# Kernel optimization log

Measured on AMD Instinct MI355X. Metric: run time of the kernel, lower is better.

Reference implementation:

```python
import jax, jax.numpy as jnp
import numpy as np

FEAT = 256
NUM_ATOMS = np.array([2048, 1536, 1024, 2048, 512, 1792, 1280, 2048], dtype=np.int32)
B = len(NUM_ATOMS)
N = int(NUM_ATOMS.sum())          # 12288 total atoms
MAXN = int(NUM_ATOMS.max())       # 2048
# Static segment bookkeeping (num_atoms is structural, not data)
_OFFSETS = np.concatenate([[0], np.cumsum(NUM_ATOMS)[:-1]])
SEG = np.repeat(np.arange(B), NUM_ATOMS)            # [N] graph id per atom
POS = np.arange(N) - _OFFSETS[SEG]                  # [N] position within graph
VALID = np.arange(MAXN)[None, :] < NUM_ATOMS[:, None]  # [B, MAXN] key mask


def setup_inputs() -> dict:
    key = jax.random.key(0)
    k1, k2 = jax.random.split(key)
    s = jax.random.normal(k1, (N, FEAT), jnp.float32)
    # dense: feat_dim -> 3*feat_dim, with bias
    W = jax.random.normal(k2, (FEAT, 3 * FEAT), jnp.float32) / np.float32(np.sqrt(FEAT))
    b = jnp.zeros((3 * FEAT,), jnp.float32)
    num_atoms = jnp.asarray(NUM_ATOMS)
    return {"s": s, "W": W, "b": b, "num_atoms": num_atoms}


def _pad(X):
    # scatter flat [N, FEAT] atoms into padded [B, MAXN, FEAT]
    return jnp.zeros((B, MAXN, FEAT), X.dtype).at[SEG, POS].set(X)


def reference(s, W, b, num_atoms):
    qkv = s @ W + b                          # [N, 3*FEAT]
    Q, K, V = jnp.split(qkv, 3, axis=-1)     # each [N, FEAT]
    Qp, Kp, Vp = _pad(Q), _pad(K), _pad(V)   # [B, MAXN, FEAT]
    scale = np.float32(1.0 / np.sqrt(FEAT))
    scores = jnp.einsum('bqd,bkd->bqk', Qp, Kp) * scale   # [B, MAXN, MAXN]
    scores = jnp.where(VALID[:, None, :], scores, -jnp.inf)  # mask padded keys
    att = jax.nn.softmax(scores, axis=-1)
    out = jnp.einsum('bqk,bkd->bqd', att, Vp)             # [B, MAXN, FEAT]
    return out[SEG, POS]                                   # back to flat [N, FEAT]
```

## Files before the change

kernel.cpp:

```cpp
#include <hip/hip_runtime.h>

typedef __attribute__((ext_vector_type(8))) short short8;
typedef __attribute__((ext_vector_type(4))) short s16x4;
typedef __attribute__((ext_vector_type(4))) float f32x4;

#define MFMA16(a,b,c) __builtin_amdgcn_mfma_f32_16x16x32_bf16((a),(b),(c),0,0,0)

__device__ __forceinline__ ushort f2bf(float f){ union{float f; unsigned u;} v; v.f=f; unsigned r=v.u + 0x7fffu + ((v.u>>16)&1u); return (ushort)(r>>16); }
__device__ __forceinline__ float bf2f(ushort u){ union{unsigned u; float f;} v; v.u = ((unsigned)u)<<16; return v.f; }

__global__ void __launch_bounds__(256) prep(const float* __restrict__ S,
    ushort* __restrict__ Sb, const float* __restrict__ W, ushort* __restrict__ Wt)
{
    __shared__ __align__(16) ushort tile[64*72];
    const int t = threadIdx.x;
    if (blockIdx.x < 1024){
        const int tid = blockIdx.x*256 + t;
#pragma unroll
        for (int r=0;r<3;r++){
            const int idx = tid + r*262144;
            f32x4 v = ((const f32x4*)S)[idx];
            s16x4 o;
            o[0]=(short)f2bf(v[0]); o[1]=(short)f2bf(v[1]);
            o[2]=(short)f2bf(v[2]); o[3]=(short)f2bf(v[3]);
            ((s16x4*)Sb)[idx] = o;
        }
    } else {
        const int i = blockIdx.x - 1024;
        const int r0 = (i&3)*64, c0 = (i>>2)*64;
        const int rr = t>>2, g = (t&3)*16;
        const float* sp = W + (size_t)(r0+rr)*768 + c0 + g;
#pragma unroll
        for (int j=0;j<16;j++) tile[(g+j)*72 + rr] = f2bf(sp[j]);
        __syncthreads();
        ushort* dp = Wt + (size_t)(c0+rr)*256 + r0 + g;
        *(short8*)dp     = *(const short8*)&tile[rr*72 + g];
        *(short8*)(dp+8) = *(const short8*)&tile[rr*72 + g + 8];
    }
}

__global__ void __launch_bounds__(256) qkv_gemm(const ushort* __restrict__ Sb,
    const ushort* __restrict__ Wt, const float* __restrict__ bias,
    ushort* __restrict__ Q, ushort* __restrict__ K, ushort* __restrict__ Vt)
{
    __shared__ __align__(16) ushort Bl[64*264];
    const int t = threadIdx.x, w = t>>6, l = t&63, lr = l&15, lq = l>>4;
    const int m0 = blockIdx.x*128, n0 = blockIdx.y*64;

    const ushort* ap = Sb + (size_t)(m0 + w*32 + lr)*256 + lq*8;
    short8 sa[2][8];
#pragma unroll
    for (int g=0;g<2;g++)
#pragma unroll
        for (int kc=0;kc<8;kc++)
            sa[g][kc] = *(const short8*)(ap + g*16*256 + kc*32);

#pragma unroll
    for (int s=0;s<8;s++){
        const int u = t + s*256, row = u>>5, c8 = u&31;
        *(short8*)&Bl[row*264 + c8*8] = *(const short8*)(Wt + (size_t)(n0+row)*256 + c8*8);
    }
    __syncthreads();

    if (n0 < 512){
        f32x4 acc[2][4];
#pragma unroll
        for (int a=0;a<2;a++)
#pragma unroll
            for (int b2=0;b2<4;b2++) acc[a][b2]=(f32x4){0.f,0.f,0.f,0.f};
#pragma unroll
        for (int kc=0;kc<8;kc++){
#pragma unroll
            for (int nt=0;nt<4;nt++){
                short8 bf = *(const short8*)&Bl[(nt*16+lr)*264 + lq*8 + kc*32];
                acc[0][nt] = MFMA16(sa[0][kc], bf, acc[0][nt]);
                acc[1][nt] = MFMA16(sa[1][kc], bf, acc[1][nt]);
            }
        }
        ushort* dst = (n0 < 256) ? Q : K;
        const int colbase = n0 & 255;
#pragma unroll
        for (int nt=0;nt<4;nt++){
            float bv = bias[n0 + nt*16 + lr];
#pragma unroll
            for (int mt=0;mt<2;mt++){
                const int row = m0 + w*32 + mt*16 + lq*4;
                ushort* o = dst + (size_t)row*256 + colbase + nt*16 + lr;
#pragma unroll
                for (int i=0;i<4;i++) o[(size_t)i*256] = f2bf(acc[mt][nt][i] + bv);
            }
        }
    } else {
        const int f0 = n0 - 512;
        f32x4 acc[4][2];
#pragma unroll
        for (int a=0;a<4;a++)
#pragma unroll
            for (int b2=0;b2<2;b2++) acc[a][b2]=(f32x4){0.f,0.f,0.f,0.f};
#pragma unroll
        for (int kc=0;kc<8;kc++){
#pragma unroll
            for (int ft=0;ft<4;ft++){
                short8 af = *(const short8*)&Bl[(ft*16+lr)*264 + lq*8 + kc*32];
                acc[ft][0] = MFMA16(af, sa[0][kc], acc[ft][0]);
                acc[ft][1] = MFMA16(af, sa[1][kc], acc[ft][1]);
            }
        }
#pragma unroll
        for (int ft=0;ft<4;ft++){
#pragma unroll
            for (int at=0;at<2;at++){
                ushort* o = Vt + (size_t)(f0 + ft*16 + lq*4)*12288 + m0 + w*32 + at*16 + lr;
#pragma unroll
                for (int i=0;i<4;i++){
                    float bv = bias[512 + f0 + ft*16 + lq*4 + i];
                    o[(size_t)i*12288] = f2bf(acc[ft][at][i] + bv);
                }
            }
        }
    }
}

template<int MODE, int PL>
__global__ void __launch_bounds__(256,2) attn_partial(const ushort* __restrict__ Qb,
    const ushort* __restrict__ Kb, const ushort* __restrict__ Vt,
    void* __restrict__ Optr, float* __restrict__ Lptr)
{
    __shared__ __align__(16) ushort Kl[32*264];
    __shared__ __align__(16) ushort Vl[256*40];
    __shared__ __align__(16) ushort Pl[4][32*40];
    const int t = threadIdx.x, w = t>>6, l = t&63, lr = l&15, lq = l>>4;
    constexpr int PIECE = 1 << PL;

    const int offs[9] = {0,2048,3584,4608,6656,7168,8960,10240,12288};
    int bi = blockIdx.x, q0=0, kstart=0, kend=0, off=0, nbg=0, pbase=0, pb=0;
#pragma unroll
    for (int s=0;s<8;s++){
        const int nb = offs[s+1]-offs[s];
        const int tiles = nb>>7, pieces = (nb + PIECE-1)>>PL;
        const int items = tiles*pieces;
        if (bi >= 0 && bi < items){
            const int tile = bi / pieces, piece = bi - tile*pieces;
            q0 = offs[s] + tile*128;
            kstart = offs[s] + piece*PIECE;
            kend = min(offs[s]+nb, kstart+PIECE);
            off = offs[s]; nbg = nb; pbase = pb;
        }
        bi -= items;
        pb += nb*pieces;
    }
    const int nchunks = (kend - kstart) >> 5;
    const int pc = (kstart - off) >> PL;

    short8 qf[2][8];
#pragma unroll
    for (int g=0;g<2;g++){
        const ushort* qp = Qb + (size_t)(q0 + w*32 + g*16 + lr)*256 + lq*8;
#pragma unroll
        for (int kc=0;kc<8;kc++) qf[g][kc] = *(const short8*)(qp + kc*32);
    }
    f32x4 Oa[2][16];
#pragma unroll
    for (int g=0;g<2;g++)
#pragma unroll
        for (int ft=0;ft<16;ft++) Oa[g][ft] = (f32x4){0.f,0.f,0.f,0.f};
    float l_lane[2][4] = {{0.f,0.f,0.f,0.f},{0.f,0.f,0.f,0.f}};

    const int kr = t>>5, kcol = t&31;
    const ushort* kg0 = Kb + (size_t)(kstart + kr)*256 + kcol*8;
    const ushort* vg0 = Vt + (size_t)t*12288 + kstart;
    short8 kreg[4], vreg[4];
#pragma unroll
    for (int s=0;s<4;s++){
        kreg[s] = *(const short8*)(kg0 + (size_t)s*8*256);
        vreg[s] = *(const short8*)(vg0 + s*8);
    }

    for (int ck=0; ck<nchunks; ck++){
#pragma unroll
        for (int s=0;s<4;s++)
            *(short8*)&Kl[(kr + s*8)*264 + kcol*8] = kreg[s];
#pragma unroll
        for (int s=0;s<4;s++)
            *(short8*)&Vl[t*40 + s*8] = vreg[s];
        if (ck+1 < nchunks){
            const ushort* kg = kg0 + (size_t)(ck+1)*32*256;
            const ushort* vg = vg0 + (ck+1)*32;
#pragma unroll
            for (int s=0;s<4;s++){
                kreg[s] = *(const short8*)(kg + (size_t)s*8*256);
                vreg[s] = *(const short8*)(vg + s*8);
            }
        }
        __syncthreads();

        f32x4 sc[2][2];
#pragma unroll
        for (int g=0;g<2;g++)
#pragma unroll
            for (int h=0;h<2;h++) sc[g][h] = (f32x4){0.f,0.f,0.f,0.f};
#pragma unroll
        for (int kc=0;kc<8;kc++){
            short8 b0 = *(const short8*)&Kl[ lr     *264 + kc*32 + lq*8];
            short8 b1 = *(const short8*)&Kl[(16+lr)*264 + kc*32 + lq*8];
#pragma unroll
            for (int g=0;g<2;g++){
                sc[g][0] = MFMA16(qf[g][kc], b0, sc[g][0]);
                sc[g][1] = MFMA16(qf[g][kc], b1, sc[g][1]);
            }
        }
        ushort* pw = &Pl[w][0];
#pragma unroll
        for (int g=0;g<2;g++)
#pragma unroll
            for (int i=0;i<4;i++){
                float p0 = exp2f(sc[g][0][i]*0.0901684284f);
                float p1 = exp2f(sc[g][1][i]*0.0901684284f);
                l_lane[g][i] += p0 + p1;
                pw[(g*16+lq*4+i)*40 + lr]      = f2bf(p0);
                pw[(g*16+lq*4+i)*40 + 16 + lr] = f2bf(p1);
            }
        __asm__ volatile("s_waitcnt lgkmcnt(0)" ::: "memory");
        short8 pf0 = *(const short8*)&pw[ lr     *40 + lq*8];
        short8 pf1 = *(const short8*)&pw[(16+lr)*40 + lq*8];

#pragma unroll
        for (int ft=0;ft<16;ft++){
            short8 vf = *(const short8*)&Vl[(ft*16+lr)*40 + lq*8];
            Oa[0][ft] = MFMA16(pf0, vf, Oa[0][ft]);
            Oa[1][ft] = MFMA16(pf1, vf, Oa[1][ft]);
        }
        __syncthreads();
    }

#pragma unroll
    for (int g=0;g<2;g++)
#pragma unroll
        for (int i=0;i<4;i++){
            float r = l_lane[g][i];
            r += __shfl_xor(r,1); r += __shfl_xor(r,2);
            r += __shfl_xor(r,4); r += __shfl_xor(r,8);
            l_lane[g][i] = r;
        }

    if constexpr (MODE == 0){
        ushort* Op = (ushort*)Optr;
        const int prow0 = pbase + pc*nbg + (q0 + w*32 - off);
#pragma unroll
        for (int g=0;g<2;g++)
#pragma unroll
            for (int i=0;i<4;i++){
                ushort* o = Op + (size_t)(prow0 + g*16 + lq*4 + i)*256 + lr;
#pragma unroll
                for (int ft=0;ft<16;ft++) o[ft*16] = f2bf(Oa[g][ft][i]);
            }
        if (lr == 0){
#pragma unroll
            for (int g=0;g<2;g++)
#pragma unroll
                for (int i=0;i<4;i++)
                    Lptr[prow0 + g*16 + lq*4 + i] = l_lane[g][i];
        }
    } else {
        float* out = (float*)Optr;
#pragma unroll
        for (int g=0;g<2;g++){
            float* op = out + (size_t)(q0 + w*32 + g*16 + lq*4)*256 + lr;
#pragma unroll
            for (int i=0;i<4;i++)
#pragma unroll
                for (int ft=0;ft<16;ft++)
                    atomicAdd(&op[(size_t)i*256 + ft*16], Oa[g][ft][i]);
        }
        if (lr == 0){
#pragma unroll
            for (int g=0;g<2;g++)
#pragma unroll
                for (int i=0;i<4;i++)
                    atomicAdd(&Lptr[q0 + w*32 + g*16 + lq*4 + i], l_lane[g][i]);
        }
    }
}

__global__ void __launch_bounds__(256) reduce_norm(const ushort* __restrict__ Opart,
    const float* __restrict__ Lpart, float* __restrict__ out, int PL)
{
    const int offs[9] = {0,2048,3584,4608,6656,7168,8960,10240,12288};
    const int t = threadIdx.x;
    const int row = blockIdx.x*8 + (t>>5);
    const int f = (t&31)*8;
    const int PIECE = 1 << PL;
    int s = 0, pbase = 0, pb = 0, nb = 0, S = 0, base = 0;
#pragma unroll
    for (int i=0;i<8;i++){
        const int nbi = offs[i+1]-offs[i];
        const int pieces = (nbi + PIECE-1) >> PL;
        if (row >= offs[i] && row < offs[i+1]){
            nb = nbi; S = pieces; pbase = pb; base = pb + (row - offs[i]);
        }
        pb += nbi*pieces;
    }
    (void)pbase; (void)s;
    float acc[8] = {0.f,0.f,0.f,0.f,0.f,0.f,0.f,0.f};
    float L = 0.f;
    for (int p=0; p<S; p++){
        const size_t pr = (size_t)(base + p*nb);
        L += Lpart[pr];
        short8 v = *(const short8*)&Opart[pr*256 + f];
#pragma unroll
        for (int j=0;j<8;j++) acc[j] += bf2f((ushort)v[j]);
    }
    const float inv = 1.0f / L;
    f32x4 o0, o1;
#pragma unroll
    for (int j=0;j<4;j++){ o0[j] = acc[j]*inv; o1[j] = acc[4+j]*inv; }
    float* op = out + (size_t)row*256 + f;
    *(f32x4*)op     = o0;
    *(f32x4*)(op+4) = o1;
}

__global__ void __launch_bounds__(256) normalize_out(float* __restrict__ out,
    const float* __restrict__ lsum)
{
    const int row = blockIdx.x, t = threadIdx.x;
    const float inv = 1.0f / lsum[row];
    out[(size_t)row*256 + t] *= inv;
}

extern "C" void kernel_launch(void* const* d_in, const int* in_sizes, int n_in,
                              void* d_out, int out_size, void* d_ws, size_t ws_size,
                              hipStream_t stream)
{
    const float* S    = nullptr;
    const float* W    = nullptr;
    const float* bias = nullptr;
    for (int i = 0; i < n_in; i++){
        if      (in_sizes[i] == 3145728) S    = (const float*)d_in[i];
        else if (in_sizes[i] ==  196608) W    = (const float*)d_in[i];
        else if (in_sizes[i] ==     768) bias = (const float*)d_in[i];
    }
    if (!S)    S    = (const float*)d_in[0];
    if (!W)    W    = (const float*)d_in[1];
    if (!bias) bias = (const float*)d_in[2];

    float* out = (float*)d_out;

    ushort* ws  = (ushort*)d_ws;
    ushort* Wt  = ws;
    ushort* Qb  = Wt + 768*256;
    ushort* Kb  = Qb + 12288*256;
    ushort* Vtb = Kb + 12288*256;

    const size_t base_b = ((size_t)768*256 + 3*(size_t)12288*256) * 2;
    const size_t need256 = base_b + (size_t)82432*512 + (size_t)82432*4;
    const size_t need512 = base_b + (size_t)42752*512 + (size_t)42752*4;

    ushort* Sb = (ushort*)d_out;

    prep     <<<1072,        256, 0, stream>>>(S, Sb, W, Wt);
    qkv_gemm <<<dim3(96,12), 256, 0, stream>>>(Sb, Wt, bias, Qb, Kb, Vtb);

    if (ws_size >= need256){
        ushort* Opart = (ushort*)((char*)d_ws + base_b);
        float*  Lpart = (float*)((char*)d_ws + base_b + (size_t)82432*512);
        attn_partial<0,8><<<644, 256, 0, stream>>>(Qb, Kb, Vtb, (void*)Opart, Lpart);
        reduce_norm      <<<1536, 256, 0, stream>>>(Opart, Lpart, out, 8);
    } else if (ws_size >= need512){
        ushort* Opart = (ushort*)((char*)d_ws + base_b);
        float*  Lpart = (float*)((char*)d_ws + base_b + (size_t)42752*512);
        attn_partial<0,9><<<334, 256, 0, stream>>>(Qb, Kb, Vtb, (void*)Opart, Lpart);
        reduce_norm      <<<1536, 256, 0, stream>>>(Opart, Lpart, out, 9);
    } else {
        float* lsum = (float*)((char*)d_ws + base_b);
        (void)hipMemsetAsync(d_out, 0, (size_t)12288*256*4, stream);
        (void)hipMemsetAsync(lsum,  0, (size_t)12288*4,     stream);
        attn_partial<1,9><<<334, 256, 0, stream>>>(Qb, Kb, Vtb, (void*)out, lsum);
        normalize_out    <<<12288, 256, 0, stream>>>(out, lsum);
    }
}
```

Measured before the change: 184.1 us.

## Build P fragments in registers via bpermute and fix key piece at 512

Swaps MFMA operand order so score tiles come out transposed, then packs exp'd probabilities to bf16 and shuffles them with ds_bpermute into the A-operand layout for the PV MFMA, removing the per-wave LDS staging buffer and its write/wait/read. Row sums now reduce across lane groups with two shuffles. The 256-wide key-piece path is dropped, so the kernel always uses 512-wide pieces with fewer blocks and less partial output to reduce. This trades LDS traffic for cross-lane permutes and fewer, larger work items.

Measured after the change: 158.7 us. 1.16x faster.

```diff
diff --git a/kernel.cpp b/kernel.cpp
--- a/kernel.cpp
+++ b/kernel.cpp
@@ -121,36 +121,34 @@
     }
 }
 
-template<int MODE, int PL>
+template<int MODE>
 __global__ void __launch_bounds__(256,2) attn_partial(const ushort* __restrict__ Qb,
     const ushort* __restrict__ Kb, const ushort* __restrict__ Vt,
     void* __restrict__ Optr, float* __restrict__ Lptr)
 {
     __shared__ __align__(16) ushort Kl[32*264];
     __shared__ __align__(16) ushort Vl[256*40];
-    __shared__ __align__(16) ushort Pl[4][32*40];
     const int t = threadIdx.x, w = t>>6, l = t&63, lr = l&15, lq = l>>4;
-    constexpr int PIECE = 1 << PL;
 
     const int offs[9] = {0,2048,3584,4608,6656,7168,8960,10240,12288};
     int bi = blockIdx.x, q0=0, kstart=0, kend=0, off=0, nbg=0, pbase=0, pb=0;
 #pragma unroll
     for (int s=0;s<8;s++){
         const int nb = offs[s+1]-offs[s];
-        const int tiles = nb>>7, pieces = (nb + PIECE-1)>>PL;
+        const int tiles = nb>>7, pieces = (nb+511)>>9;
         const int items = tiles*pieces;
         if (bi >= 0 && bi < items){
             const int tile = bi / pieces, piece = bi - tile*pieces;
             q0 = offs[s] + tile*128;
-            kstart = offs[s] + piece*PIECE;
-            kend = min(offs[s]+nb, kstart+PIECE);
+            kstart = offs[s] + piece*512;
+            kend = min(offs[s]+nb, kstart+512);
             off = offs[s]; nbg = nb; pbase = pb;
         }
         bi -= items;
         pb += nb*pieces;
     }
     const int nchunks = (kend - kstart) >> 5;
-    const int pc = (kstart - off) >> PL;
+    const int pc = (kstart - off) >> 9;
 
     short8 qf[2][8];
 #pragma unroll
@@ -164,7 +162,7 @@
     for (int g=0;g<2;g++)
 #pragma unroll
         for (int ft=0;ft<16;ft++) Oa[g][ft] = (f32x4){0.f,0.f,0.f,0.f};
-    float l_lane[2][4] = {{0.f,0.f,0.f,0.f},{0.f,0.f,0.f,0.f}};
+    float l_lane[2] = {0.f, 0.f};
 
     const int kr = t>>5, kcol = t&31;
     const ushort* kg0 = Kb + (size_t)(kstart + kr)*256 + kcol*8;
@@ -175,6 +173,10 @@
         kreg[s] = *(const short8*)(kg0 + (size_t)s*8*256);
         vreg[s] = *(const short8*)(vg0 + s*8);
     }
+
+    const int i0 = 4*(lr + 32*(lq&1));
+    const int i1 = i0 + 64;
+    const bool hi = (lq >= 2);
 
     for (int ck=0; ck<nchunks; ck++){
 #pragma unroll
@@ -196,52 +198,67 @@
 
         f32x4 sc[2][2];
 #pragma unroll
-        for (int g=0;g<2;g++)
-#pragma unroll
-            for (int h=0;h<2;h++) sc[g][h] = (f32x4){0.f,0.f,0.f,0.f};
+        for (int h=0;h<2;h++)
+#pragma unroll
+            for (int g=0;g<2;g++) sc[h][g] = (f32x4){0.f,0.f,0.f,0.f};
 #pragma unroll
         for (int kc=0;kc<8;kc++){
             short8 b0 = *(const short8*)&Kl[ lr     *264 + kc*32 + lq*8];
             short8 b1 = *(const short8*)&Kl[(16+lr)*264 + kc*32 + lq*8];
 #pragma unroll
             for (int g=0;g<2;g++){
-                sc[g][0] = MFMA16(qf[g][kc], b0, sc[g][0]);
-                sc[g][1] = MFMA16(qf[g][kc], b1, sc[g][1]);
-            }
-        }
-        ushort* pw = &Pl[w][0];
-#pragma unroll
-        for (int g=0;g<2;g++)
-#pragma unroll
-            for (int i=0;i<4;i++){
-                float p0 = exp2f(sc[g][0][i]*0.0901684284f);
-                float p1 = exp2f(sc[g][1][i]*0.0901684284f);
-                l_lane[g][i] += p0 + p1;
-                pw[(g*16+lq*4+i)*40 + lr]      = f2bf(p0);
-                pw[(g*16+lq*4+i)*40 + 16 + lr] = f2bf(p1);
-            }
-        __asm__ volatile("s_waitcnt lgkmcnt(0)" ::: "memory");
-        short8 pf0 = *(const short8*)&pw[ lr     *40 + lq*8];
-        short8 pf1 = *(const short8*)&pw[(16+lr)*40 + lq*8];
+                sc[0][g] = MFMA16(b0, qf[g][kc], sc[0][g]);
+                sc[1][g] = MFMA16(b1, qf[g][kc], sc[1][g]);
+            }
+        }
+
+        short8 pa[2];
+#pragma unroll
+        for (int g=0;g<2;g++){
+            float p[8];
+#pragma unroll
+            for (int h=0;h<2;h++)
+#pragma unroll
+                for (int i=0;i<4;i++){
+                    float v = exp2f(sc[h][g][i]*0.0901684284f);
+                    p[h*4+i] = v;
+                    l_lane[g] += v;
+                }
+            unsigned w0 = (unsigned)f2bf(p[0]) | ((unsigned)f2bf(p[1])<<16);
+            unsigned w1 = (unsigned)f2bf(p[2]) | ((unsigned)f2bf(p[3])<<16);
+            unsigned w2 = (unsigned)f2bf(p[4]) | ((unsigned)f2bf(p[5])<<16);
+            unsigned w3 = (unsigned)f2bf(p[6]) | ((unsigned)f2bf(p[7])<<16);
+            unsigned a0 = (unsigned)__builtin_amdgcn_ds_bpermute(i0, (int)w0);
+            unsigned a2 = (unsigned)__builtin_amdgcn_ds_bpermute(i0, (int)w2);
+            unsigned b1w= (unsigned)__builtin_amdgcn_ds_bpermute(i0, (int)w1);
+            unsigned b3 = (unsigned)__builtin_amdgcn_ds_bpermute(i0, (int)w3);
+            unsigned c0 = (unsigned)__builtin_amdgcn_ds_bpermute(i1, (int)w0);
+            unsigned c2 = (unsigned)__builtin_amdgcn_ds_bpermute(i1, (int)w2);
+            unsigned d1 = (unsigned)__builtin_amdgcn_ds_bpermute(i1, (int)w1);
+            unsigned d3 = (unsigned)__builtin_amdgcn_ds_bpermute(i1, (int)w3);
+            union { unsigned u[4]; short8 s8; } pk;
+            pk.u[0] = hi ? a2 : a0;
+            pk.u[1] = hi ? b3 : b1w;
+            pk.u[2] = hi ? c2 : c0;
+            pk.u[3] = hi ? d3 : d1;
+            pa[g] = pk.s8;
+        }
 
 #pragma unroll
         for (int ft=0;ft<16;ft++){
             short8 vf = *(const short8*)&Vl[(ft*16+lr)*40 + lq*8];
-            Oa[0][ft] = MFMA16(pf0, vf, Oa[0][ft]);
-            Oa[1][ft] = MFMA16(pf1, vf, Oa[1][ft]);
+            Oa[0][ft] = MFMA16(pa[0], vf, Oa[0][ft]);
+            Oa[1][ft] = MFMA16(pa[1], vf, Oa[1][ft]);
         }
         __syncthreads();
     }
 
 #pragma unroll
-    for (int g=0;g<2;g++)
-#pragma unroll
-        for (int i=0;i<4;i++){
-            float r = l_lane[g][i];
-            r += __shfl_xor(r,1); r += __shfl_xor(r,2);
-            r += __shfl_xor(r,4); r += __shfl_xor(r,8);
-            l_lane[g][i] = r;
-        }
+    for (int g=0;g<2;g++){
+        float r = l_lane[g];
+        r += __shfl_xor(r,16); r += __shfl_xor(r,32);
+        l_lane[g] = r;
+    }
 
     if constexpr (MODE == 0){
         ushort* Op = (ushort*)Optr;
@@ -254,12 +271,9 @@
 #pragma unroll
                 for (int ft=0;ft<16;ft++) o[ft*16] = f2bf(Oa[g][ft][i]);
             }
-        if (lr == 0){
-#pragma unroll
-            for (int g=0;g<2;g++)
-#pragma unroll
-                for (int i=0;i<4;i++)
-                    Lptr[prow0 + g*16 + lq*4 + i] = l_lane[g][i];
+        if (l < 16){
+            Lptr[prow0 + lr]      = l_lane[0];
+            Lptr[prow0 + 16 + lr] = l_lane[1];
         }
     } else {
         float* out = (float*)Optr;
@@ -272,12 +286,9 @@
                 for (int ft=0;ft<16;ft++)
                     atomicAdd(&op[(size_t)i*256 + ft*16], Oa[g][ft][i]);
         }
-        if (lr == 0){
-#pragma unroll
-            for (int g=0;g<2;g++)
-#pragma unroll
-                for (int i=0;i<4;i++)
-                    atomicAdd(&Lptr[q0 + w*32 + g*16 + lq*4 + i], l_lane[g][i]);
+        if (l < 16){
+            atomicAdd(&Lptr[q0 + w*32 + lr],      l_lane[0]);
+            atomicAdd(&Lptr[q0 + w*32 + 16 + lr], l_lane[1]);
         }
     }
 }
@@ -290,17 +301,16 @@
     const int row = blockIdx.x*8 + (t>>5);
     const int f = (t&31)*8;
     const int PIECE = 1 << PL;
-    int s = 0, pbase = 0, pb = 0, nb = 0, S = 0, base = 0;
+    int pb = 0, nb = 0, S = 0, base = 0;
 #pragma unroll
     for (int i=0;i<8;i++){
         const int nbi = offs[i+1]-offs[i];
         const int pieces = (nbi + PIECE-1) >> PL;
         if (row >= offs[i] && row < offs[i+1]){
-            nb = nbi; S = pieces; pbase = pb; base = pb + (row - offs[i]);
+            nb = nbi; S = pieces; base = pb + (row - offs[i]);
         }
         pb += nbi*pieces;
     }
-    (void)pbase; (void)s;
     float acc[8] = {0.f,0.f,0.f,0.f,0.f,0.f,0.f,0.f};
     float L = 0.f;
     for (int p=0; p<S; p++){
@@ -351,8 +361,7 @@
     ushort* Kb  = Qb + 12288*256;
     ushort* Vtb = Kb + 12288*256;
 
-    const size_t base_b = ((size_t)768*256 + 3*(size_t)12288*256) * 2;
-    const size_t need256 = base_b + (size_t)82432*512 + (size_t)82432*4;
+    const size_t base_b  = ((size_t)768*256 + 3*(size_t)12288*256) * 2;
     const size_t need512 = base_b + (size_t)42752*512 + (size_t)42752*4;
 
     ushort* Sb = (ushort*)d_out;
@@ -360,21 +369,16 @@
     prep     <<<1072,        256, 0, stream>>>(S, Sb, W, Wt);
     qkv_gemm <<<dim3(96,12), 256, 0, stream>>>(Sb, Wt, bias, Qb, Kb, Vtb);
 
-    if (ws_size >= need256){
-        ushort* Opart = (ushort*)((char*)d_ws + base_b);
-        float*  Lpart = (float*)((char*)d_ws + base_b + (size_t)82432*512);
-        attn_partial<0,8><<<644, 256, 0, stream>>>(Qb, Kb, Vtb, (void*)Opart, Lpart);
-        reduce_norm      <<<1536, 256, 0, stream>>>(Opart, Lpart, out, 8);
-    } else if (ws_size >= need512){
+    if (ws_size >= need512){
         ushort* Opart = (ushort*)((char*)d_ws + base_b);
         float*  Lpart = (float*)((char*)d_ws + base_b + (size_t)42752*512);
-        attn_partial<0,9><<<334, 256, 0, stream>>>(Qb, Kb, Vtb, (void*)Opart, Lpart);
-        reduce_norm      <<<1536, 256, 0, stream>>>(Opart, Lpart, out, 9);
+        attn_partial<0><<<334, 256, 0, stream>>>(Qb, Kb, Vtb, (void*)Opart, Lpart);
+        reduce_norm    <<<1536, 256, 0, stream>>>(Opart, Lpart, out, 9);
     } else {
         float* lsum = (float*)((char*)d_ws + base_b);
         (void)hipMemsetAsync(d_out, 0, (size_t)12288*256*4, stream);
         (void)hipMemsetAsync(lsum,  0, (size_t)12288*4,     stream);
-        attn_partial<1,9><<<334, 256, 0, stream>>>(Qb, Kb, Vtb, (void*)out, lsum);
-        normalize_out    <<<12288, 256, 0, stream>>>(out, lsum);
-    }
-}
+        attn_partial<1><<<334, 256, 0, stream>>>(Qb, Kb, Vtb, (void*)out, lsum);
+        normalize_out  <<<12288, 256, 0, stream>>>(out, lsum);
+    }
+}
```
